# Performance work log

Measured on AMD Instinct MI355X. Metric: run time of the kernel, lower is better.

## Reference

```python
import jax, jax.numpy as jnp
import numpy as np
from jax import lax

DIM = 64
B, H, W = 4, 256, 256


def setup_inputs() -> dict:
    key = jax.random.key(0)
    ks = jax.random.split(key, 6)
    d = DIM
    x = jax.random.normal(ks[0], (B, d, H, W), dtype=jnp.float32)
    w_hidden = jax.random.normal(ks[1], (6 * d, d), dtype=jnp.float32) * 0.05      # 1x1 conv dim->6*dim
    w_dw = jax.random.normal(ks[2], (6 * d, 1, 3, 3), dtype=jnp.float32) * 0.05    # depthwise 3x3
    norm_w = jnp.ones((2 * d,), dtype=jnp.float32)
    norm_b = jnp.zeros((2 * d,), dtype=jnp.float32)
    w_out = jax.random.normal(ks[3], (d, 2 * d), dtype=jnp.float32) * 0.05         # 1x1 conv 2*dim->dim
    return {"x": x, "w_hidden": w_hidden, "w_dw": w_dw,
            "norm_w": norm_w, "norm_b": norm_b, "w_out": w_out, "patch_size": 8}


def reference(x, w_hidden, w_dw, norm_w, norm_b, w_out, patch_size):
    p = patch_size
    b, c, h, w = x.shape
    # 1x1 conv: dim -> 6*dim
    hidden = jnp.einsum('oc,bchw->bohw', w_hidden, x)
    # depthwise 3x3 conv, padding=1
    hidden = lax.conv_general_dilated(
        hidden, w_dw, window_strides=(1, 1), padding='SAME',
        dimension_numbers=('NCHW', 'OIHW', 'NCHW'),
        feature_group_count=w_dw.shape[0])
    q, k, v = jnp.split(hidden, 3, axis=1)  # each [b, 2c, h, w]

    c2 = 2 * c
    def to_patch(t):  # b c (h p1) (w p2) -> b c h w p1 p2
        return t.reshape(b, c2, h // p, p, w // p, p).transpose(0, 1, 2, 4, 3, 5)

    q_fft = jnp.fft.rfft2(to_patch(q).astype(jnp.float32))
    k_fft = jnp.fft.rfft2(to_patch(k).astype(jnp.float32))
    out = jnp.fft.irfft2(q_fft * k_fft, s=(p, p))  # circular conv per patch
    # b c h w p1 p2 -> b c (h p1) (w p2)
    out = out.transpose(0, 1, 2, 4, 3, 5).reshape(b, c2, h, w)

    # WithBias LayerNorm over channel dim (to_3d normalizes last dim = channels)
    mu = out.mean(axis=1, keepdims=True)
    var = out.var(axis=1, keepdims=True)
    out_norm = (out - mu) / jnp.sqrt(var + 1e-5)
    out_norm = out_norm * norm_w[None, :, None, None] + norm_b[None, :, None, None]

    gated = v * out_norm
    # 1x1 conv: 2*dim -> dim
    return jnp.einsum('oc,bchw->bohw', w_out, gated)
```

## Files before the change

kernel.cpp:

```cpp
#include <hip/hip_runtime.h>


typedef _Float16 f16x8 __attribute__((ext_vector_type(8)));
typedef _Float16 f16x4 __attribute__((ext_vector_type(4)));
typedef _Float16 f16x2 __attribute__((ext_vector_type(2)));
typedef __fp16   h16x2 __attribute__((ext_vector_type(2)));
typedef float    f32x4 __attribute__((ext_vector_type(4)));

#define XS_OFF    0
#define HS_OFF    15232
#define QCC_OFF   28800
#define TMP_OFF   63616
#define MU_OFF    72832
#define S2_OFF    73088
#define LNW_OFF   73344
#define LNB_OFF   73856
#define LDS_BYTES 74368

__global__ __launch_bounds__(512, 4) void lfsa_fused(
    const float* __restrict__ x,
    const float* __restrict__ wh,
    const float* __restrict__ wdw,
    const float* __restrict__ nw,
    const float* __restrict__ nb,
    const float* __restrict__ wo,
    float* __restrict__ out)
{
    extern __shared__ char lds[];
    _Float16* xs    = (_Float16*)(lds + XS_OFF);
    _Float16* hs    = (_Float16*)(lds + HS_OFF);
    float*    qcc   = (float*)(lds + QCC_OFF);
    _Float16* tmp16 = (_Float16*)(lds + TMP_OFF);
    _Float16* gs16  = (_Float16*)(lds + TMP_OFF);
    float*    mu_s  = (float*)(lds + MU_OFF);
    float*    s2_s  = (float*)(lds + S2_OFF);
    float*    lnw   = (float*)(lds + LNW_OFF);
    float*    lnb   = (float*)(lds + LNB_OFF);

    const int tid = threadIdx.x;
    const int px = blockIdx.x, py = blockIdx.y, bz = blockIdx.z;
    const int lane = tid & 63;
    const int wv   = tid >> 6;
    const int m16  = lane & 15;
    const int quad = lane >> 4;

    {
        const int pix = tid & 127;
        const int gg  = tid >> 7;
        const int prow = pix / 10;
        const int pcol = pix - prow * 10;
        const int yy = py * 8 + prow - 1;
        const int xx = px * 8 + pcol - 1;
        const bool inimg = (pix < 100) && ((unsigned)yy < 256u) && ((unsigned)xx < 256u);
        if (pix < 112) {
            const float* xp = inimg
                ? (x + (size_t)((bz * 64 + gg * 16) * 65536 + yy * 256 + xx)) : x;
            #pragma unroll
            for (int i = 0; i < 16; ++i) {
                const float v = inimg ? xp[(size_t)i * 65536] : 0.0f;
                xs[pix * 68 + gg * 16 + i] = (_Float16)v;
            }
        }
        if (tid < 128) { lnw[tid] = nw[tid]; lnb[tid] = nb[tid]; }
    }

    const int dwo = tid >> 3;
    const int blk = tid & 7;
    const int by2 = (blk >> 1) * 2;
    const int bx4 = (blk & 1) * 4;
    const int ci  = tid & 7;

    const int ot = wv >> 1;
    const float* wha = wh + (size_t)(ot * 16 + m16) * 64 + quad * 8;
    float4 wr0 = *(const float4*)(wha);
    float4 wr1 = *(const float4*)(wha + 4);
    float4 wr2 = *(const float4*)(wha + 32);
    float4 wr3 = *(const float4*)(wha + 36);
    float w9n[9];
    #pragma unroll
    for (int t = 0; t < 9; ++t) w9n[t] = wdw[dwo * 9 + t];
    float4 wo0, wo1, wo2, wo3;

    f32x4 pacc2[2] = {{0.f,0.f,0.f,0.f},{0.f,0.f,0.f,0.f}};

    __syncthreads();

    #pragma unroll 1
    for (int kc = 0; kc < 6; ++kc) {
        const f16x8 a0 = {(_Float16)wr0.x,(_Float16)wr0.y,(_Float16)wr0.z,(_Float16)wr0.w,
                          (_Float16)wr1.x,(_Float16)wr1.y,(_Float16)wr1.z,(_Float16)wr1.w};
        const f16x8 a1 = {(_Float16)wr2.x,(_Float16)wr2.y,(_Float16)wr2.z,(_Float16)wr2.w,
                          (_Float16)wr3.x,(_Float16)wr3.y,(_Float16)wr3.z,(_Float16)wr3.w};
        float w9c[9];
        #pragma unroll
        for (int t = 0; t < 9; ++t) w9c[t] = w9n[t];
        if (kc < 5) {
            const float* nx = wha + (size_t)(kc + 1) * 4096;
            wr0 = *(const float4*)(nx);
            wr1 = *(const float4*)(nx + 4);
            wr2 = *(const float4*)(nx + 32);
            wr3 = *(const float4*)(nx + 36);
            #pragma unroll
            for (int t = 0; t < 9; ++t) w9n[t] = wdw[(kc + 1) * 576 + dwo * 9 + t];
        }
        if (kc == 3) {
            const float* wop = wo + (size_t)(ot * 16 + m16) * 128 + quad * 8;
            wo0 = *(const float4*)(wop);
            wo1 = *(const float4*)(wop + 4);
            wo2 = *(const float4*)(wop + 32);
            wo3 = *(const float4*)(wop + 36);
        }

        {
            const int np  = (wv & 1) ? 3 : 4;
            const int pt0 = (wv & 1) * 4;
            for (int pp = 0; pp < np; ++pp) {
                const int pt = pt0 + pp;
                const _Float16* bp = xs + (pt * 16 + m16) * 68 + quad * 8;
                const f16x4 bl0 = *(const f16x4*)bp;
                const f16x4 bh0 = *(const f16x4*)(bp + 4);
                const f16x4 bl1 = *(const f16x4*)(bp + 32);
                const f16x4 bh1 = *(const f16x4*)(bp + 36);
                const f16x8 b0 = {bl0[0],bl0[1],bl0[2],bl0[3],bh0[0],bh0[1],bh0[2],bh0[3]};
                const f16x8 b1 = {bl1[0],bl1[1],bl1[2],bl1[3],bh1[0],bh1[1],bh1[2],bh1[3]};
                f32x4 d = {0.f,0.f,0.f,0.f};
                d = __builtin_amdgcn_mfma_f32_16x16x32_f16(a0, b0, d, 0, 0, 0);
                d = __builtin_amdgcn_mfma_f32_16x16x32_f16(a1, b1, d, 0, 0, 0);
                const int pixg = pt * 16 + m16;
                if (pixg < 100) {
                    const int oloc = ot * 16 + quad * 4;
                    #pragma unroll
                    for (int r = 0; r < 4; ++r)
                        hs[106 * (oloc + r) + pixg] = (_Float16)d[r];
                }
            }
        }
        __syncthreads();

        if (kc < 4) {
            const _Float16* hrow = hs + 106 * dwo;
            float in[4][6];
            #pragma unroll
            for (int r = 0; r < 4; ++r) {
                const _Float16* rp = hrow + (by2 + r) * 10 + bx4;
                const f16x2 p0 = *(const f16x2*)rp;
                const f16x2 p1 = *(const f16x2*)(rp + 2);
                const f16x2 p2 = *(const f16x2*)(rp + 4);
                in[r][0] = (float)p0[0]; in[r][1] = (float)p0[1];
                in[r][2] = (float)p1[0]; in[r][3] = (float)p1[1];
                in[r][4] = (float)p2[0]; in[r][5] = (float)p2[1];
            }
            #pragma unroll
            for (int r = 0; r < 2; ++r) {
                float rv[4];
                #pragma unroll
                for (int c = 0; c < 4; ++c) {
                    float s = 0.0f;
                    #pragma unroll
                    for (int dy = 0; dy < 3; ++dy)
                        #pragma unroll
                        for (int dx = 0; dx < 3; ++dx)
                            s = fmaf(w9c[dy * 3 + dx], in[r + dy][c + dx], s);
                    rv[c] = s;
                }
                const int off = (by2 + r) * 8 + bx4;
                if (kc < 2) {
                    float* qrow = qcc + 68 * (kc * 64 + dwo);
                    *(f32x4*)(qrow + off) = {rv[0], rv[1], rv[2], rv[3]};
                } else {
                    _Float16* trow = tmp16 + 72 * dwo;
                    *(f16x4*)(trow + off) = f16x4{(_Float16)rv[0], (_Float16)rv[1],
                                                  (_Float16)rv[2], (_Float16)rv[3]};
                }
            }
        } else {
            const _Float16* hrow = hs + 106 * dwo;
            float c0[10], c1[10], c2[10];
            #pragma unroll
            for (int rr = 0; rr < 10; ++rr) {
                c0[rr] = (float)hrow[rr * 10 + blk];
                c1[rr] = (float)hrow[rr * 10 + blk + 1];
                c2[rr] = (float)hrow[rr * 10 + blk + 2];
            }
            #pragma unroll
            for (int r = 0; r < 8; ++r) {
                float s = 0.0f;
                #pragma unroll
                for (int dy = 0; dy < 3; ++dy) {
                    s = fmaf(w9c[dy * 3 + 0], c0[r + dy], s);
                    s = fmaf(w9c[dy * 3 + 1], c1[r + dy], s);
                    s = fmaf(w9c[dy * 3 + 2], c2[r + dy], s);
                }
                gs16[(r * 8 + blk) * 72 + dwo] = (_Float16)s;
            }
        }
        __syncthreads();

        if (kc == 2 || kc == 3) {
            const int ch = (kc - 2) * 64 + dwo;
            float* qrow = qcc + 68 * ch;
            const _Float16* krow = tmp16 + 72 * dwo;
            float acc[8];
            #pragma unroll
            for (int j = 0; j < 8; ++j) acc[j] = 0.0f;
            #pragma unroll
            for (int a = 0; a < 8; ++a) {
                const f32x4 qa = *(const f32x4*)(qrow + 8 * a);
                const f32x4 qb = *(const f32x4*)(qrow + 8 * a + 4);
                h16x2 q2[4];
                q2[0] = __builtin_amdgcn_cvt_pkrtz(qa[0], qa[1]);
                q2[1] = __builtin_amdgcn_cvt_pkrtz(qa[2], qa[3]);
                q2[2] = __builtin_amdgcn_cvt_pkrtz(qb[0], qb[1]);
                q2[3] = __builtin_amdgcn_cvt_pkrtz(qb[2], qb[3]);
                const int r = (ci - a) & 7;
                const f16x8 kr = *(const f16x8*)(krow + 8 * r);
                h16x2 rp[8];
                #pragma unroll
                for (int i = 0; i < 8; ++i)
                    rp[i] = h16x2{(__fp16)kr[i], (__fp16)kr[(i + 7) & 7]};
                #pragma unroll
                for (int j = 0; j < 8; ++j)
                    #pragma unroll
                    for (int t = 0; t < 4; ++t)
                        acc[j] = __builtin_amdgcn_fdot2(q2[t], rp[(j - 2 * t) & 7],
                                                        acc[j], false);
            }
            *(f32x4*)(qrow + 8 * ci)     = {acc[0], acc[1], acc[2], acc[3]};
            *(f32x4*)(qrow + 8 * ci + 4) = {acc[4], acc[5], acc[6], acc[7]};
        }

        if (kc == 3) {
            __syncthreads();
            const int p = 8 * wv + (lane & 7);
            const int g = lane >> 3;
            float s = 0.0f, s2v = 0.0f;
            #pragma unroll
            for (int i = 0; i < 16; ++i) {
                const float v = qcc[68 * (g + 8 * i) + p];
                s += v; s2v = fmaf(v, v, s2v);
            }
            #pragma unroll
            for (int m = 8; m < 64; m <<= 1) {
                s   += __shfl_xor(s, m, 64);
                s2v += __shfl_xor(s2v, m, 64);
            }
            if (lane < 8) {
                mu_s[p] = s * (1.0f / 128.0f);
                s2_s[p] = s2v * (1.0f / 128.0f);
            }
        }

        if (kc >= 4) {
            const int p  = tid & 63;
            const int g8 = wv;
            const int cb = (kc - 4) * 64;
            const float m    = mu_s[p];
            const float rstd = rsqrtf(s2_s[p] - m * m + 1e-5f);
            const f16x8 vv = *(const f16x8*)(gs16 + p * 72 + g8 * 8);
            f16x8 gv;
            #pragma unroll
            for (int jj = 0; jj < 8; ++jj) {
                const int chl = g8 * 8 + jj;
                const float c0 = qcc[68 * (cb + chl) + p];
                gv[jj] = (_Float16)((float)vv[jj] *
                         ((c0 - m) * rstd * lnw[cb + chl] + lnb[cb + chl]));
            }
            *(f16x8*)(gs16 + p * 72 + g8 * 8) = gv;
            __syncthreads();
            const f16x8 pa0 = {(_Float16)wo0.x,(_Float16)wo0.y,(_Float16)wo0.z,(_Float16)wo0.w,
                               (_Float16)wo1.x,(_Float16)wo1.y,(_Float16)wo1.z,(_Float16)wo1.w};
            const f16x8 pa1 = {(_Float16)wo2.x,(_Float16)wo2.y,(_Float16)wo2.z,(_Float16)wo2.w,
                               (_Float16)wo3.x,(_Float16)wo3.y,(_Float16)wo3.z,(_Float16)wo3.w};
            #pragma unroll
            for (int tt = 0; tt < 2; ++tt) {
                const int pt = (wv & 1) * 2 + tt;
                const _Float16* bp = gs16 + (pt * 16 + m16) * 72 + quad * 8;
                const f16x8 b0 = *(const f16x8*)bp;
                const f16x8 b1 = *(const f16x8*)(bp + 32);
                pacc2[tt] = __builtin_amdgcn_mfma_f32_16x16x32_f16(pa0, b0, pacc2[tt], 0, 0, 0);
                pacc2[tt] = __builtin_amdgcn_mfma_f32_16x16x32_f16(pa1, b1, pacc2[tt], 0, 0, 0);
            }
            if (kc == 4) {
                const float* wop = wo + (size_t)(ot * 16 + m16) * 128 + 64 + quad * 8;
                wo0 = *(const float4*)(wop);
                wo1 = *(const float4*)(wop + 4);
                wo2 = *(const float4*)(wop + 32);
                wo3 = *(const float4*)(wop + 36);
            }
        }
    }

    {
        #pragma unroll
        for (int tt = 0; tt < 2; ++tt) {
            const int pixg = ((wv & 1) * 2 + tt) * 16 + m16;
            const int r = pixg >> 3, c = pixg & 7;
            float* op = out + (size_t)(bz * 64 + ot * 16 + quad * 4) * 65536
                            + (py * 8 + r) * 256 + px * 8 + c;
            #pragma unroll
            for (int reg = 0; reg < 4; ++reg)
                op[(size_t)reg * 65536] = pacc2[tt][reg];
        }
    }
}

extern "C" void kernel_launch(void* const* d_in, const int* in_sizes, int n_in,
                              void* d_out, int out_size, void* d_ws, size_t ws_size,
                              hipStream_t stream) {
    const float* x   = (const float*)d_in[0];
    const float* wh  = (const float*)d_in[1];
    const float* wdw = (const float*)d_in[2];
    const float* nw  = (const float*)d_in[3];
    const float* nb  = (const float*)d_in[4];
    const float* wo  = (const float*)d_in[5];
    float* outp = (float*)d_out;

    (void)hipFuncSetAttribute((const void*)lfsa_fused,
                              hipFuncAttributeMaxDynamicSharedMemorySize, LDS_BYTES);
    dim3 grid(32, 32, 4);
    lfsa_fused<<<grid, 512, LDS_BYTES, stream>>>(x, wh, wdw, nw, nb, wo, outp);
}
```

Before: 412.3 us.

## Shrink LDS with fp16 buffers, swizzle x tile, fuse LayerNorm gating into depthwise

Stores the q/correlation buffer and LayerNorm weights in fp16 instead of fp32. It also packs the hidden and x tiles more tightly, using an XOR swizzle on the x tile so it can be read with wide vector loads, and raises the launch bound from 4 to 6 blocks per CU. The LayerNorm normalize-and-gate step moves into the v depthwise loop and rstd is computed once per pixel, which removes a separate pass and a barrier. The extra occupancy is meant to hide latency. In exchange, the correlation outputs are rounded to fp16 before the LayerNorm statistics, and the unpadded strides of 100 and 68 may cause LDS bank conflicts.

After: 677.7 us. 64.4% more time.

```diff
diff --git a/kernel.cpp b/kernel.cpp
--- a/kernel.cpp
+++ b/kernel.cpp
@@ -8,16 +8,16 @@
 typedef float    f32x4 __attribute__((ext_vector_type(4)));
 
 #define XS_OFF    0
-#define HS_OFF    15232
-#define QCC_OFF   28800
-#define TMP_OFF   63616
-#define MU_OFF    72832
-#define S2_OFF    73088
-#define LNW_OFF   73344
-#define LNB_OFF   73856
-#define LDS_BYTES 74368
-
-__global__ __launch_bounds__(512, 4) void lfsa_fused(
+#define HS_OFF    14336
+#define QCC_OFF   27136
+#define TMP_OFF   44544
+#define MU_OFF    53248
+#define RSTD_OFF  53504
+#define LNW_OFF   53760
+#define LNB_OFF   54016
+#define LDS_BYTES 54272
+
+__global__ __launch_bounds__(512, 6) void lfsa_fused(
     const float* __restrict__ x,
     const float* __restrict__ wh,
     const float* __restrict__ wdw,
@@ -29,13 +29,13 @@
     extern __shared__ char lds[];
     _Float16* xs    = (_Float16*)(lds + XS_OFF);
     _Float16* hs    = (_Float16*)(lds + HS_OFF);
-    float*    qcc   = (float*)(lds + QCC_OFF);
+    _Float16* qcc16 = (_Float16*)(lds + QCC_OFF);
     _Float16* tmp16 = (_Float16*)(lds + TMP_OFF);
     _Float16* gs16  = (_Float16*)(lds + TMP_OFF);
     float*    mu_s  = (float*)(lds + MU_OFF);
-    float*    s2_s  = (float*)(lds + S2_OFF);
-    float*    lnw   = (float*)(lds + LNW_OFF);
-    float*    lnb   = (float*)(lds + LNB_OFF);
+    float*    rstd_s= (float*)(lds + RSTD_OFF);
+    _Float16* lnw16 = (_Float16*)(lds + LNW_OFF);
+    _Float16* lnb16 = (_Float16*)(lds + LNB_OFF);
 
     const int tid = threadIdx.x;
     const int px = blockIdx.x, py = blockIdx.y, bz = blockIdx.z;
@@ -45,8 +45,8 @@
     const int quad = lane >> 4;
 
     {
-        const int pix = tid & 127;
-        const int gg  = tid >> 7;
+        const int pix  = tid & 127;
+        const int gg   = tid >> 7;
         const int prow = pix / 10;
         const int pcol = pix - prow * 10;
         const int yy = py * 8 + prow - 1;
@@ -55,13 +55,18 @@
         if (pix < 112) {
             const float* xp = inimg
                 ? (x + (size_t)((bz * 64 + gg * 16) * 65536 + yy * 256 + xx)) : x;
-            #pragma unroll
-            for (int i = 0; i < 16; ++i) {
-                const float v = inimg ? xp[(size_t)i * 65536] : 0.0f;
-                xs[pix * 68 + gg * 16 + i] = (_Float16)v;
-            }
-        }
-        if (tid < 128) { lnw[tid] = nw[tid]; lnb[tid] = nb[tid]; }
+            f16x8 lo, hi;
+            #pragma unroll
+            for (int i = 0; i < 8; ++i) {
+                lo[i] = (_Float16)(inimg ? xp[(size_t)i * 65536] : 0.0f);
+                hi[i] = (_Float16)(inimg ? xp[(size_t)(i + 8) * 65536] : 0.0f);
+            }
+            const int s = pix & 7;
+            _Float16* xrow = xs + pix * 64;
+            *(f16x8*)(xrow + (((2 * gg)     ^ s) * 8)) = lo;
+            *(f16x8*)(xrow + (((2 * gg + 1) ^ s) * 8)) = hi;
+        }
+        if (tid < 128) { lnw16[tid] = (_Float16)nw[tid]; lnb16[tid] = (_Float16)nb[tid]; }
     }
 
     const int dwo = tid >> 3;
@@ -116,29 +121,26 @@
             const int pt0 = (wv & 1) * 4;
             for (int pp = 0; pp < np; ++pp) {
                 const int pt = pt0 + pp;
-                const _Float16* bp = xs + (pt * 16 + m16) * 68 + quad * 8;
-                const f16x4 bl0 = *(const f16x4*)bp;
-                const f16x4 bh0 = *(const f16x4*)(bp + 4);
-                const f16x4 bl1 = *(const f16x4*)(bp + 32);
-                const f16x4 bh1 = *(const f16x4*)(bp + 36);
-                const f16x8 b0 = {bl0[0],bl0[1],bl0[2],bl0[3],bh0[0],bh0[1],bh0[2],bh0[3]};
-                const f16x8 b1 = {bl1[0],bl1[1],bl1[2],bl1[3],bh1[0],bh1[1],bh1[2],bh1[3]};
+                const int pixg = pt * 16 + m16;
+                const _Float16* xrow = xs + pixg * 64;
+                const int c0 = ((quad ^ (pixg & 7)) * 8);
+                const f16x8 b0 = *(const f16x8*)(xrow + c0);
+                const f16x8 b1 = *(const f16x8*)(xrow + (c0 ^ 32));
                 f32x4 d = {0.f,0.f,0.f,0.f};
                 d = __builtin_amdgcn_mfma_f32_16x16x32_f16(a0, b0, d, 0, 0, 0);
                 d = __builtin_amdgcn_mfma_f32_16x16x32_f16(a1, b1, d, 0, 0, 0);
-                const int pixg = pt * 16 + m16;
                 if (pixg < 100) {
                     const int oloc = ot * 16 + quad * 4;
                     #pragma unroll
                     for (int r = 0; r < 4; ++r)
-                        hs[106 * (oloc + r) + pixg] = (_Float16)d[r];
+                        hs[100 * (oloc + r) + pixg] = (_Float16)d[r];
                 }
             }
         }
         __syncthreads();
 
         if (kc < 4) {
-            const _Float16* hrow = hs + 106 * dwo;
+            const _Float16* hrow = hs + 100 * dwo;
             float in[4][6];
             #pragma unroll
             for (int r = 0; r < 4; ++r) {
@@ -164,17 +166,13 @@
                     rv[c] = s;
                 }
                 const int off = (by2 + r) * 8 + bx4;
-                if (kc < 2) {
-                    float* qrow = qcc + 68 * (kc * 64 + dwo);
-                    *(f32x4*)(qrow + off) = {rv[0], rv[1], rv[2], rv[3]};
-                } else {
-                    _Float16* trow = tmp16 + 72 * dwo;
-                    *(f16x4*)(trow + off) = f16x4{(_Float16)rv[0], (_Float16)rv[1],
-                                                  (_Float16)rv[2], (_Float16)rv[3]};
-                }
+                _Float16* dst = (kc < 2) ? (qcc16 + 68 * (kc * 64 + dwo))
+                                         : (tmp16 + 68 * dwo);
+                *(f16x4*)(dst + off) = f16x4{(_Float16)rv[0], (_Float16)rv[1],
+                                             (_Float16)rv[2], (_Float16)rv[3]};
             }
         } else {
-            const _Float16* hrow = hs + 106 * dwo;
+            const _Float16* hrow = hs + 100 * dwo;
             float c0[10], c1[10], c2[10];
             #pragma unroll
             for (int rr = 0; rr < 10; ++rr) {
@@ -182,6 +180,9 @@
                 c1[rr] = (float)hrow[rr * 10 + blk + 1];
                 c2[rr] = (float)hrow[rr * 10 + blk + 2];
             }
+            const int chg = (kc - 4) * 64 + dwo;
+            const float lw = (float)lnw16[chg], lb = (float)lnb16[chg];
+            const _Float16* ccrow = qcc16 + 68 * chg;
             #pragma unroll
             for (int r = 0; r < 8; ++r) {
                 float s = 0.0f;
@@ -191,27 +192,28 @@
                     s = fmaf(w9c[dy * 3 + 1], c1[r + dy], s);
                     s = fmaf(w9c[dy * 3 + 2], c2[r + dy], s);
                 }
-                gs16[(r * 8 + blk) * 72 + dwo] = (_Float16)s;
-            }
-        }
-        __syncthreads();
+                const int p = r * 8 + blk;
+                const float nrm = ((float)ccrow[p] - mu_s[p]) * rstd_s[p] * lw + lb;
+                gs16[p * 68 + dwo] = (_Float16)(s * nrm);
+            }
+        }
 
         if (kc == 2 || kc == 3) {
             const int ch = (kc - 2) * 64 + dwo;
-            float* qrow = qcc + 68 * ch;
-            const _Float16* krow = tmp16 + 72 * dwo;
+            _Float16* qrow = qcc16 + 68 * ch;
+            const _Float16* krow = tmp16 + 68 * dwo;
             float acc[8];
             #pragma unroll
             for (int j = 0; j < 8; ++j) acc[j] = 0.0f;
             #pragma unroll
             for (int a = 0; a < 8; ++a) {
-                const f32x4 qa = *(const f32x4*)(qrow + 8 * a);
-                const f32x4 qb = *(const f32x4*)(qrow + 8 * a + 4);
+                const f16x8 qv = *(const f16x8*)(qrow + 8 * a);
                 h16x2 q2[4];
-                q2[0] = __builtin_amdgcn_cvt_pkrtz(qa[0], qa[1]);
-                q2[1] = __builtin_amdgcn_cvt_pkrtz(qa[2], qa[3]);
-                q2[2] = __builtin_amdgcn_cvt_pkrtz(qb[0], qb[1]);
-                q2[3] = __builtin_amdgcn_cvt_pkrtz(qb[2], qb[3]);
+                #pragma unroll
+                for (int t = 0; t < 4; ++t) {
+                    q2[t][0] = (__fp16)qv[2 * t];
+                    q2[t][1] = (__fp16)qv[2 * t + 1];
+                }
                 const int r = (ci - a) & 7;
                 const f16x8 kr = *(const f16x8*)(krow + 8 * r);
                 h16x2 rp[8];
@@ -225,18 +227,20 @@
                         acc[j] = __builtin_amdgcn_fdot2(q2[t], rp[(j - 2 * t) & 7],
                                                         acc[j], false);
             }
-            *(f32x4*)(qrow + 8 * ci)     = {acc[0], acc[1], acc[2], acc[3]};
-            *(f32x4*)(qrow + 8 * ci + 4) = {acc[4], acc[5], acc[6], acc[7]};
-        }
+            *(f16x4*)(qrow + 8 * ci)     = f16x4{(_Float16)acc[0], (_Float16)acc[1],
+                                                 (_Float16)acc[2], (_Float16)acc[3]};
+            *(f16x4*)(qrow + 8 * ci + 4) = f16x4{(_Float16)acc[4], (_Float16)acc[5],
+                                                 (_Float16)acc[6], (_Float16)acc[7]};
+        }
+        __syncthreads();
 
         if (kc == 3) {
-            __syncthreads();
             const int p = 8 * wv + (lane & 7);
             const int g = lane >> 3;
             float s = 0.0f, s2v = 0.0f;
             #pragma unroll
             for (int i = 0; i < 16; ++i) {
-                const float v = qcc[68 * (g + 8 * i) + p];
+                const float v = (float)qcc16[68 * (g + 8 * i) + p];
                 s += v; s2v = fmaf(v, v, s2v);
             }
             #pragma unroll
@@ -245,28 +249,13 @@
                 s2v += __shfl_xor(s2v, m, 64);
             }
             if (lane < 8) {
-                mu_s[p] = s * (1.0f / 128.0f);
-                s2_s[p] = s2v * (1.0f / 128.0f);
+                const float mu = s * (1.0f / 128.0f);
+                mu_s[p]   = mu;
+                rstd_s[p] = rsqrtf(s2v * (1.0f / 128.0f) - mu * mu + 1e-5f);
             }
         }
 
         if (kc >= 4) {
-            const int p  = tid & 63;
-            const int g8 = wv;
-            const int cb = (kc - 4) * 64;
-            const float m    = mu_s[p];
-            const float rstd = rsqrtf(s2_s[p] - m * m + 1e-5f);
-            const f16x8 vv = *(const f16x8*)(gs16 + p * 72 + g8 * 8);
-            f16x8 gv;
-            #pragma unroll
-            for (int jj = 0; jj < 8; ++jj) {
-                const int chl = g8 * 8 + jj;
-                const float c0 = qcc[68 * (cb + chl) + p];
-                gv[jj] = (_Float16)((float)vv[jj] *
-                         ((c0 - m) * rstd * lnw[cb + chl] + lnb[cb + chl]));
-            }
-            *(f16x8*)(gs16 + p * 72 + g8 * 8) = gv;
-            __syncthreads();
             const f16x8 pa0 = {(_Float16)wo0.x,(_Float16)wo0.y,(_Float16)wo0.z,(_Float16)wo0.w,
                                (_Float16)wo1.x,(_Float16)wo1.y,(_Float16)wo1.z,(_Float16)wo1.w};
             const f16x8 pa1 = {(_Float16)wo2.x,(_Float16)wo2.y,(_Float16)wo2.z,(_Float16)wo2.w,
@@ -274,7 +263,7 @@
             #pragma unroll
             for (int tt = 0; tt < 2; ++tt) {
                 const int pt = (wv & 1) * 2 + tt;
-                const _Float16* bp = gs16 + (pt * 16 + m16) * 72 + quad * 8;
+                const _Float16* bp = gs16 + (pt * 16 + m16) * 68 + quad * 8;
                 const f16x8 b0 = *(const f16x8*)bp;
                 const f16x8 b1 = *(const f16x8*)(bp + 32);
                 pacc2[tt] = __builtin_amdgcn_mfma_f32_16x16x32_f16(pa0, b0, pacc2[tt], 0, 0, 0);
```
